# Kernel optimization log

Measured on AMD Instinct MI355X. Metric: run time of the kernel, lower is better.

Reference implementation:

```python
import jax, jax.numpy as jnp
import numpy as np

N_NODES = 50000
N_EDGES = 1600000
IN_FEATS = 256
OUT_FEATS = 128
NEG_SLOPE = 0.2


def setup_inputs() -> dict:
    key = jax.random.key(0)
    k1, k2, k3, k4, k5, k6 = jax.random.split(key, 6)
    gain = np.sqrt(2.0)  # calculate_gain('relu')
    w_std = gain * np.sqrt(2.0 / (IN_FEATS + OUT_FEATS))  # xavier normal
    a_std = gain * np.sqrt(2.0 / (1 + OUT_FEATS))
    return {
        "feat": jax.random.normal(k1, (N_NODES, IN_FEATS), dtype=jnp.float32),
        "W": jax.random.normal(k2, (OUT_FEATS, IN_FEATS), dtype=jnp.float32) * w_std,
        "attn_l": jax.random.normal(k3, (1, OUT_FEATS), dtype=jnp.float32) * a_std,
        "attn_r": jax.random.normal(k4, (1, OUT_FEATS), dtype=jnp.float32) * a_std,
        "src": jax.random.randint(k5, (N_EDGES,), 0, N_NODES, dtype=jnp.int32),
        "dst": jax.random.randint(k6, (N_EDGES,), 0, N_NODES, dtype=jnp.int32),
    }


def reference(feat, W, attn_l, attn_r, src, dst):
    # h = fc(feat): [N, D]
    h = jnp.einsum("ni,di->nd", feat, W)
    # per-node attention logits
    el = jnp.sum(h * attn_l, axis=-1)  # [N]
    er = jnp.sum(h * attn_r, axis=-1)  # [N]
    # apply_edge: e_uv = el[u] + er[v], then leaky relu
    e = jax.nn.leaky_relu(el[src] + er[dst], NEG_SLOPE)  # [E]
    # edge softmax over incoming edges of each destination node
    m = jax.ops.segment_max(e, dst, num_segments=N_NODES)  # [N]
    m = jnp.where(jnp.isneginf(m), 0.0, m)  # nodes with no in-edges
    ex = jnp.exp(e - m[dst])  # [E]
    denom = jax.ops.segment_sum(ex, dst, num_segments=N_NODES)  # [N]
    alpha = ex / jnp.maximum(denom[dst], 1e-9)  # [E]
    # gspmv: rst[v] = sum_{(u->v)} alpha_uv * h[u]
    rst = jax.ops.segment_sum(h[src] * alpha[:, None], dst, num_segments=N_NODES)
    return rst
```

## Files before the change

kernel.cpp:

```cpp
#include <hip/hip_runtime.h>
#include <hip/hip_bf16.h>


#define IN_FEATS 256
#define OUT_FEATS 128
#define NBINS 1024
#define BUCK 64
#define CAPB_LOG 12
#define CAPB (1 << CAPB_LOG)
#define SORT_CAP 8192
#define SCAT_BLOCKS 256
#define BIN_STRIDE 16

typedef __bf16 bf16x8 __attribute__((ext_vector_type(8)));
typedef float f32x4 __attribute__((ext_vector_type(4)));

__global__ void prep(const float* __restrict__ W, __bf16* __restrict__ Wb, int nw,
                     int* __restrict__ cur) {
    int i = blockIdx.x * 256 + threadIdx.x;
    if (i < nw) Wb[i] = (__bf16)W[i];
    if (i < NBINS) cur[i * BIN_STRIDE] = i << CAPB_LOG;
}

__global__ __launch_bounds__(512) void gemm_scatter(
    const float* __restrict__ feat, const __bf16* __restrict__ Wb,
    const float* __restrict__ attn_l, const float* __restrict__ attn_r,
    __bf16* __restrict__ hb, float* __restrict__ el, float* __restrict__ er,
    const int* __restrict__ src, const int* __restrict__ dst,
    int* __restrict__ bin_cur, unsigned* __restrict__ arena,
    int n, int E, int S) {
    __shared__ unsigned sorted[SORT_CAP];
    __shared__ int h[NBINS];
    __shared__ int off[NBINS];
    __shared__ int gbase[NBINS];

    if (blockIdx.x < S) {
        const int t = threadIdx.x;
        const int t2 = t + 512;
        const int chunk = (E + S - 1) / S;
        const int beg = blockIdx.x * chunk;
        const int end = min(beg + chunk, E);

        h[t] = 0; h[t2] = 0;
        __syncthreads();
        for (int i = beg + t; i < end; i += 512)
            atomicAdd(&h[dst[i] >> 6], 1);
        __syncthreads();

        off[t] = h[t]; off[t2] = h[t2];
        __syncthreads();
        for (int o = 1; o < NBINS; o <<= 1) {
            int v0 = (t >= o) ? off[t - o] : 0;
            int v1 = (t2 >= o) ? off[t2 - o] : 0;
            __syncthreads();
            off[t] += v0; off[t2] += v1;
            __syncthreads();
        }
        const int c0 = h[t], c1 = h[t2];
        const int e0 = off[t] - c0, e1 = off[t2] - c1;
        __syncthreads();
        off[t] = e0; off[t2] = e1;
        if (c0 > 0) gbase[t] = atomicAdd(&bin_cur[t * BIN_STRIDE], c0);
        if (c1 > 0) gbase[t2] = atomicAdd(&bin_cur[t2 * BIN_STRIDE], c1);
        h[t] = 0; h[t2] = 0;
        __syncthreads();

        for (int i = beg + t; i < end; i += 512) {
            int d = dst[i];
            int bin = d >> 6;
            int r = atomicAdd(&h[bin], 1);
            sorted[off[bin] + r] = ((unsigned)d << 16) | (unsigned)src[i];
        }
        __syncthreads();

        const int tot = end - beg;
        for (int j = t; j < tot; j += 512) {
            unsigned w = sorted[j];
            int bin = w >> 22;
            int pos = gbase[bin] + (j - off[bin]);
            pos = min(pos, ((bin + 1) << CAPB_LOG) - 1);
            arena[pos] = w;
        }
        return;
    }

    const int wid = threadIdx.x >> 6;
    const int lane = threadIdx.x & 63;
    const int s = lane & 15;
    const int q = lane >> 4;
    const int m0 = (blockIdx.x - S) * 128 + wid * 16;
    if (m0 >= n) return;

    const int mrow = min(m0 + s, n - 1);
    const float* arow = feat + (size_t)mrow * IN_FEATS + q * 8;

    f32x4 acc[8];
#pragma unroll
    for (int nt = 0; nt < 8; nt++) acc[nt] = (f32x4){0.f, 0.f, 0.f, 0.f};

#pragma unroll
    for (int ks = 0; ks < 8; ks++) {
        const int k0 = ks * 32;
        float4 f0 = *(const float4*)(arow + k0);
        float4 f1 = *(const float4*)(arow + k0 + 4);
        bf16x8 a;
        a[0] = (__bf16)f0.x; a[1] = (__bf16)f0.y; a[2] = (__bf16)f0.z; a[3] = (__bf16)f0.w;
        a[4] = (__bf16)f1.x; a[5] = (__bf16)f1.y; a[6] = (__bf16)f1.z; a[7] = (__bf16)f1.w;
#pragma unroll
        for (int nt = 0; nt < 8; nt++) {
            bf16x8 b = *(const bf16x8*)(Wb + (size_t)(nt * 16 + s) * IN_FEATS + k0 + q * 8);
            acc[nt] = __builtin_amdgcn_mfma_f32_16x16x32_bf16(a, b, acc[nt], 0, 0, 0);
        }
    }

    float al[8], ar[8];
#pragma unroll
    for (int nt = 0; nt < 8; nt++) {
        al[nt] = attn_l[nt * 16 + s];
        ar[nt] = attn_r[nt * 16 + s];
    }

#pragma unroll
    for (int r = 0; r < 4; r++) {
        const int row = m0 + q * 4 + r;
        const bool ok = row < n;
        float pl = 0.f, pr = 0.f;
#pragma unroll
        for (int nt = 0; nt < 8; nt++) {
            float v = acc[nt][r];
            if (ok) hb[(size_t)row * OUT_FEATS + nt * 16 + s] = (__bf16)v;
            pl += v * al[nt];
            pr += v * ar[nt];
        }
#pragma unroll
        for (int m = 1; m < 16; m <<= 1) {
            pl += __shfl_xor(pl, m);
            pr += __shfl_xor(pr, m);
        }
        if (ok && s == 0) {
            el[row] = pl;
            er[row] = pr;
        }
    }
}

__global__ __launch_bounds__(512) void csr_gat(
    const unsigned* __restrict__ arena, const int* __restrict__ bin_cur,
    const float* __restrict__ el, const float* __restrict__ er,
    const __bf16* __restrict__ hb, float* __restrict__ out, int N) {
    __shared__ unsigned stage[CAPB];
    __shared__ int cnt[BUCK];
    __shared__ int off[BUCK];
    __shared__ float erl[BUCK];
    const int b = blockIdx.x;
    const int t = threadIdx.x;
    const int abeg = b << CAPB_LOG;
    const int cin = min(bin_cur[b * BIN_STRIDE] - abeg, CAPB);
    const int d0 = b * BUCK;

    if (t < BUCK) {
        cnt[t] = 0;
        erl[t] = (d0 + t < N) ? er[d0 + t] : 0.f;
    }
    __syncthreads();

    for (int i = t; i < cin; i += 512)
        atomicAdd(&cnt[(arena[abeg + i] >> 16) & (BUCK - 1)], 1);
    __syncthreads();
    if (t < BUCK) off[t] = cnt[t];
    __syncthreads();
    for (int o = 1; o < BUCK; o <<= 1) {
        int v = (t < BUCK && t >= o) ? off[t - o] : 0;
        __syncthreads();
        if (t < BUCK) off[t] += v;
        __syncthreads();
    }
    if (t < BUCK) {
        off[t] -= cnt[t];
        cnt[t] = 0;
    }
    __syncthreads();

    for (int i = t; i < cin; i += 512) {
        unsigned e = arena[abeg + i];
        int d6 = (e >> 16) & (BUCK - 1);
        int u = (int)(e & 0xFFFFu);
        float x = el[u] + erl[d6];
        x = (x > 0.f) ? x : 0.2f * x;
        float w = __expf(x);
        int r = atomicAdd(&cnt[d6], 1);
        stage[off[d6] + r] = (__float_as_uint(w) & 0xFFFF0000u) | (unsigned)u;
    }
    __syncthreads();

    const int wid = t >> 6;
    const int lane = t & 63;
    const unsigned* hbu = (const unsigned*)hb;
#pragma unroll 1
    for (int j = 0; j < BUCK / 8; j++) {
        const int d6 = wid * (BUCK / 8) + j;
        const int v = d0 + d6;
        if (v >= N) break;
        const int rbeg = __builtin_amdgcn_readfirstlane(off[d6]);
        const int deg  = __builtin_amdgcn_readfirstlane(cnt[d6]);
        float acc0 = 0.f, acc1 = 0.f, wsum = 0.f;
        for (int c0 = rbeg; c0 < rbeg + deg; c0 += 64) {
            const int nn = min(64, rbeg + deg - c0);
            unsigned my = (lane < nn) ? stage[c0 + lane] : 0u;
            int k = 0;
            for (; k + 8 <= nn; k += 8) {
#pragma unroll
                for (int tt = 0; tt < 8; tt++) {
                    const unsigned es = (unsigned)__builtin_amdgcn_readlane((int)my, k + tt);
                    const unsigned us = es & 0xFFFFu;
                    const float ws = __uint_as_float(es & 0xFFFF0000u);
                    const unsigned pair = hbu[(size_t)us * (OUT_FEATS / 2) + lane];
                    wsum += ws;
                    acc0 += ws * __uint_as_float(pair << 16);
                    acc1 += ws * __uint_as_float(pair & 0xffff0000u);
                }
            }
            for (; k < nn; k++) {
                const unsigned es = (unsigned)__builtin_amdgcn_readlane((int)my, k);
                const unsigned us = es & 0xFFFFu;
                const float ws = __uint_as_float(es & 0xFFFF0000u);
                const unsigned pair = hbu[(size_t)us * (OUT_FEATS / 2) + lane];
                wsum += ws;
                acc0 += ws * __uint_as_float(pair << 16);
                acc1 += ws * __uint_as_float(pair & 0xffff0000u);
            }
        }
        const float dnm = fmaxf(wsum, 1e-9f);
        float2 o = make_float2(acc0 / dnm, acc1 / dnm);
        *(float2*)(out + (size_t)v * OUT_FEATS + lane * 2) = o;
    }
}

extern "C" void kernel_launch(void* const* d_in, const int* in_sizes, int n_in,
                              void* d_out, int out_size, void* d_ws, size_t ws_size,
                              hipStream_t stream) {
    const float* feat   = (const float*)d_in[0];
    const float* W      = (const float*)d_in[1];
    const float* attn_l = (const float*)d_in[2];
    const float* attn_r = (const float*)d_in[3];
    const int*   src    = (const int*)d_in[4];
    const int*   dst    = (const int*)d_in[5];
    const int N = in_sizes[0] / IN_FEATS;
    const int E = in_sizes[4];
    float* out = (float*)d_out;

    char* p = (char*)d_ws;
    auto alloc = [&](size_t bytes) -> char* {
        char* r = p;
        p += (bytes + 255) & ~(size_t)255;
        return r;
    };
    const int nbuckets = (N + BUCK - 1) / BUCK;

    __bf16* hb      = (__bf16*)alloc((size_t)N * OUT_FEATS * sizeof(__bf16));
    __bf16* Wb      = (__bf16*)alloc((size_t)OUT_FEATS * IN_FEATS * sizeof(__bf16));
    float*  el      = (float*)alloc((size_t)N * sizeof(float));
    float*  er      = (float*)alloc((size_t)N * sizeof(float));
    int*    bin_cur = (int*)alloc((size_t)NBINS * BIN_STRIDE * sizeof(int));
    unsigned* arena = (unsigned*)alloc((size_t)NBINS * CAPB * sizeof(unsigned));

    const int nw = OUT_FEATS * IN_FEATS;
    prep<<<dim3((nw + 255) / 256), dim3(256), 0, stream>>>(W, Wb, nw, bin_cur);

    const int G = (N + 127) / 128;
    gemm_scatter<<<dim3(SCAT_BLOCKS + G), dim3(512), 0, stream>>>(
        feat, Wb, attn_l, attn_r, hb, el, er, src, dst, bin_cur, arena, N, E,
        SCAT_BLOCKS);

    csr_gat<<<dim3(nbuckets), dim3(512), 0, stream>>>(arena, bin_cur, el, er,
                                                      hb, out, N);
}
```

Baseline: 220.7 us.

## Shrink fused gemm/scatter blocks to 256 threads and put GEMM blocks first

Halves the block size of the fused GEMM+edge-bucketing kernel to 256 threads and doubles the number of scatter blocks, so each scatter block sorts half as many edges in a smaller LDS buffer. The 1024-bin prefix scan becomes a per-thread 4-bin sum followed by a 256-wide scan, and GEMM blocks are now ordered before scatter blocks in the grid. The aim is lower LDS per block for higher occupancy and better mixing of the two block types. In exchange there are twice as many global atomics on the bin cursors and more scatter blocks, each with fewer edges.

```diff
diff --git a/kernel.cpp b/kernel.cpp
--- a/kernel.cpp
+++ b/kernel.cpp
@@ -8,8 +8,8 @@
 #define BUCK 64
 #define CAPB_LOG 12
 #define CAPB (1 << CAPB_LOG)
-#define SORT_CAP 8192
-#define SCAT_BLOCKS 256
+#define SORT_CAP 4096
+#define SCAT_BLOCKS 512
 #define BIN_STRIDE 16
 
 typedef __bf16 bf16x8 __attribute__((ext_vector_type(8)));
@@ -22,50 +22,55 @@
     if (i < NBINS) cur[i * BIN_STRIDE] = i << CAPB_LOG;
 }
 
-__global__ __launch_bounds__(512) void gemm_scatter(
+__global__ __launch_bounds__(256) void gemm_scatter(
     const float* __restrict__ feat, const __bf16* __restrict__ Wb,
     const float* __restrict__ attn_l, const float* __restrict__ attn_r,
     __bf16* __restrict__ hb, float* __restrict__ el, float* __restrict__ er,
     const int* __restrict__ src, const int* __restrict__ dst,
     int* __restrict__ bin_cur, unsigned* __restrict__ arena,
-    int n, int E, int S) {
+    int n, int E, int G) {
     __shared__ unsigned sorted[SORT_CAP];
     __shared__ int h[NBINS];
     __shared__ int off[NBINS];
     __shared__ int gbase[NBINS];
-
-    if (blockIdx.x < S) {
+    __shared__ int sblk[256];
+
+    if (blockIdx.x >= G) {
         const int t = threadIdx.x;
-        const int t2 = t + 512;
-        const int chunk = (E + S - 1) / S;
-        const int beg = blockIdx.x * chunk;
+        const int blk = blockIdx.x - G;
+        const int chunk = (E + SCAT_BLOCKS - 1) / SCAT_BLOCKS;
+        const int beg = blk * chunk;
         const int end = min(beg + chunk, E);
 
-        h[t] = 0; h[t2] = 0;
-        __syncthreads();
-        for (int i = beg + t; i < end; i += 512)
+        h[4 * t] = 0; h[4 * t + 1] = 0; h[4 * t + 2] = 0; h[4 * t + 3] = 0;
+        __syncthreads();
+        for (int i = beg + t; i < end; i += 256)
             atomicAdd(&h[dst[i] >> 6], 1);
         __syncthreads();
 
-        off[t] = h[t]; off[t2] = h[t2];
-        __syncthreads();
-        for (int o = 1; o < NBINS; o <<= 1) {
-            int v0 = (t >= o) ? off[t - o] : 0;
-            int v1 = (t2 >= o) ? off[t2 - o] : 0;
+        const int a0 = h[4 * t], a1 = h[4 * t + 1], a2 = h[4 * t + 2], a3 = h[4 * t + 3];
+        const int tot = a0 + a1 + a2 + a3;
+        sblk[t] = tot;
+        __syncthreads();
+        for (int o = 1; o < 256; o <<= 1) {
+            int v = (t >= o) ? sblk[t - o] : 0;
             __syncthreads();
-            off[t] += v0; off[t2] += v1;
+            sblk[t] += v;
             __syncthreads();
         }
-        const int c0 = h[t], c1 = h[t2];
-        const int e0 = off[t] - c0, e1 = off[t2] - c1;
-        __syncthreads();
-        off[t] = e0; off[t2] = e1;
-        if (c0 > 0) gbase[t] = atomicAdd(&bin_cur[t * BIN_STRIDE], c0);
-        if (c1 > 0) gbase[t2] = atomicAdd(&bin_cur[t2 * BIN_STRIDE], c1);
-        h[t] = 0; h[t2] = 0;
-        __syncthreads();
-
-        for (int i = beg + t; i < end; i += 512) {
+        const int base = sblk[t] - tot;
+        off[4 * t] = base;
+        off[4 * t + 1] = base + a0;
+        off[4 * t + 2] = base + a0 + a1;
+        off[4 * t + 3] = base + a0 + a1 + a2;
+        if (a0 > 0) gbase[4 * t]     = atomicAdd(&bin_cur[(4 * t) * BIN_STRIDE], a0);
+        if (a1 > 0) gbase[4 * t + 1] = atomicAdd(&bin_cur[(4 * t + 1) * BIN_STRIDE], a1);
+        if (a2 > 0) gbase[4 * t + 2] = atomicAdd(&bin_cur[(4 * t + 2) * BIN_STRIDE], a2);
+        if (a3 > 0) gbase[4 * t + 3] = atomicAdd(&bin_cur[(4 * t + 3) * BIN_STRIDE], a3);
+        h[4 * t] = 0; h[4 * t + 1] = 0; h[4 * t + 2] = 0; h[4 * t + 3] = 0;
+        __syncthreads();
+
+        for (int i = beg + t; i < end; i += 256) {
             int d = dst[i];
             int bin = d >> 6;
             int r = atomicAdd(&h[bin], 1);
@@ -73,8 +78,8 @@
         }
         __syncthreads();
 
-        const int tot = end - beg;
-        for (int j = t; j < tot; j += 512) {
+        const int tot2 = end - beg;
+        for (int j = t; j < tot2; j += 256) {
             unsigned w = sorted[j];
             int bin = w >> 22;
             int pos = gbase[bin] + (j - off[bin]);
@@ -88,7 +93,7 @@
     const int lane = threadIdx.x & 63;
     const int s = lane & 15;
     const int q = lane >> 4;
-    const int m0 = (blockIdx.x - S) * 128 + wid * 16;
+    const int m0 = blockIdx.x * 64 + wid * 16;
     if (m0 >= n) return;
 
     const int mrow = min(m0 + s, n - 1);
@@ -267,10 +272,9 @@
     const int nw = OUT_FEATS * IN_FEATS;
     prep<<<dim3((nw + 255) / 256), dim3(256), 0, stream>>>(W, Wb, nw, bin_cur);
 
-    const int G = (N + 127) / 128;
-    gemm_scatter<<<dim3(SCAT_BLOCKS + G), dim3(512), 0, stream>>>(
-        feat, Wb, attn_l, attn_r, hb, el, er, src, dst, bin_cur, arena, N, E,
-        SCAT_BLOCKS);
+    const int G = (N + 63) / 64;
+    gemm_scatter<<<dim3(G + SCAT_BLOCKS), dim3(256), 0, stream>>>(
+        feat, Wb, attn_l, attn_r, hb, el, er, src, dst, bin_cur, arena, N, E, G);
 
     csr_gat<<<dim3(nbuckets), dim3(512), 0, stream>>>(arena, bin_cur, el, er,
                                                       hb, out, N);
```

Result: no change. 218.6 us (-0.9%).
